# Kernel tuning notes

Hardware: AMD Instinct MI355X
Metric: run time of the kernel (lower is better)

Reference implementation:

```python
import jax, jax.numpy as jnp
import numpy as np


def setup_inputs() -> dict:
    key = jax.random.key(0)
    k1, k2, k3 = jax.random.split(key, 3)
    B, H, W, C, Q = 32, 64, 64, 256, 4
    h = jax.random.normal(k1, (B, H, W, C), dtype=jnp.float32)
    mask = jax.random.randint(k2, (B, H, W), 0, 2) == 1  # True = masked out
    queries = jax.random.normal(k3, (Q, C), dtype=jnp.float32)
    return {"h": h, "mask": mask, "queries": queries}


def reference(h, mask, queries):
    B, H, W, C = h.shape
    Q = queries.shape[0]
    scale = C ** (-0.5)
    h_flat = h.reshape(B, H * W, C)            # [B, N, C]
    # scores: [B, Q, N]
    attn = jnp.einsum('qc,bnc->bqn', queries, h_flat) * scale
    mask_flat = mask.reshape(B, 1, H * W)      # True -> -inf
    attn = jnp.where(mask_flat, -jnp.inf, attn)
    attn = jax.nn.softmax(attn, axis=-1)
    attn = jnp.where(jnp.isnan(attn), 0.0, attn)  # nan_to_num for fully-masked rows
    pooled = jnp.einsum('bqn,bnc->bqc', attn, h_flat)
    return pooled.reshape(B, Q * C)
```

## Files before the change

### kernel.cpp

```cpp
#include <hip/hip_runtime.h>
#include <math.h>

#define QN  4
#define CN  256
#define BN  32
#define NN  4096
#define WV  4
#define RPW 64
#define TR  8
#define NT  8
#define SPB 16

#define LOADT(tt) do {                                                   \
    _Pragma("unroll")                                                    \
    for (int j_ = 0; j_ < TR; ++j_) {                                    \
        const int rw_ = (tt) * TR + j_;                                  \
        if (!((mbits >> rw_) & 1ull))                                    \
            vst[j_] = *(const float4*)(hb + (size_t)rw_ * CN + lane * 4);\
        else                                                             \
            vst[j_] = make_float4(0.f, 0.f, 0.f, 0.f);                   \
    }                                                                    \
} while (0)

#define STORET(bp) do {                                                  \
    _Pragma("unroll")                                                    \
    for (int j_ = 0; j_ < TR; ++j_)                                      \
        *(float4*)((bp) + j_ * CN + lane * 4) = vst[j_];                 \
} while (0)

__global__ __launch_bounds__(256) void k_fused(
    const float* __restrict__ h, const int* __restrict__ mask,
    const float* __restrict__ qr,
    float* __restrict__ P, float* __restrict__ L)
{
    __shared__ float  s_stage[WV][2][TR * CN];
    __shared__ float4 s_pb[WV][TR];
    __shared__ float  s_lp[WV][QN];

    const int b    = blockIdx.x >> 4;
    const int sub  = blockIdx.x & (SPB - 1);
    const int w    = threadIdx.x >> 6;
    const int lane = threadIdx.x & 63;
    const int rgrp = lane >> 4;
    const int l15  = lane & 15;

    const int n0    = (sub * WV + w) * RPW;
    const size_t gn = (size_t)b * NN + n0;
    const float* __restrict__ hb = h + gn * CN;

    float4 q4[QN][4];
#pragma unroll
    for (int q = 0; q < QN; ++q)
#pragma unroll
        for (int k = 0; k < 4; ++k) {
            float4 t = *(const float4*)(qr + q * CN + (l15 + 16 * k) * 4);
            t.x *= 0.0625f; t.y *= 0.0625f; t.z *= 0.0625f; t.w *= 0.0625f;
            q4[q][k] = t;
        }

    const unsigned long long mbits = __ballot(mask[gn + lane] != 0);

    float* const buf0 = &s_stage[w][0][0];
    float* const buf1 = &s_stage[w][1][0];

    float4 acc[QN];
    float  lsum[QN];
#pragma unroll
    for (int q = 0; q < QN; ++q) {
        acc[q] = make_float4(0.f, 0.f, 0.f, 0.f);
        lsum[q] = 0.f;
    }

    float4 vst[TR];

    LOADT(0);
    STORET(buf0);
    LOADT(1);

    for (int t = 0; t < NT; ++t) {
        float* const bufc = (t & 1) ? buf1 : buf0;
        float* const bufn = (t & 1) ? buf0 : buf1;

#pragma unroll
        for (int sp = 0; sp < 2; ++sp) {
            const int rt = sp * 4 + rgrp;
            const float* rowp = bufc + rt * CN;
            float s0 = 0.f, s1 = 0.f, s2 = 0.f, s3 = 0.f;
#pragma unroll
            for (int k = 0; k < 4; ++k) {
                const float4 hv = *(const float4*)(rowp + (l15 + 16 * k) * 4);
                s0 += hv.x * q4[0][k].x + hv.y * q4[0][k].y
                    + hv.z * q4[0][k].z + hv.w * q4[0][k].w;
                s1 += hv.x * q4[1][k].x + hv.y * q4[1][k].y
                    + hv.z * q4[1][k].z + hv.w * q4[1][k].w;
                s2 += hv.x * q4[2][k].x + hv.y * q4[2][k].y
                    + hv.z * q4[2][k].z + hv.w * q4[2][k].w;
                s3 += hv.x * q4[3][k].x + hv.y * q4[3][k].y
                    + hv.z * q4[3][k].z + hv.w * q4[3][k].w;
            }
#pragma unroll
            for (int off = 1; off <= 8; off <<= 1) {
                s0 += __shfl_xor(s0, off, 64);
                s1 += __shfl_xor(s1, off, 64);
                s2 += __shfl_xor(s2, off, 64);
                s3 += __shfl_xor(s3, off, 64);
            }
            const bool mk = ((mbits >> (t * TR + rt)) & 1ull) != 0;
            float4 pv;
            pv.x = mk ? 0.f : __expf(s0);
            pv.y = mk ? 0.f : __expf(s1);
            pv.z = mk ? 0.f : __expf(s2);
            pv.w = mk ? 0.f : __expf(s3);
            if (l15 == 0) s_pb[w][rt] = pv;
        }

#pragma unroll
        for (int r = 0; r < TR; ++r) {
            const float4 pv = s_pb[w][r];
            const float4 hv = *(const float4*)(bufc + r * CN + lane * 4);
            acc[0].x += pv.x * hv.x; acc[0].y += pv.x * hv.y;
            acc[0].z += pv.x * hv.z; acc[0].w += pv.x * hv.w;
            acc[1].x += pv.y * hv.x; acc[1].y += pv.y * hv.y;
            acc[1].z += pv.y * hv.z; acc[1].w += pv.y * hv.w;
            acc[2].x += pv.z * hv.x; acc[2].y += pv.z * hv.y;
            acc[2].z += pv.z * hv.z; acc[2].w += pv.z * hv.w;
            acc[3].x += pv.w * hv.x; acc[3].y += pv.w * hv.y;
            acc[3].z += pv.w * hv.z; acc[3].w += pv.w * hv.w;
            lsum[0] += pv.x; lsum[1] += pv.y;
            lsum[2] += pv.z; lsum[3] += pv.w;
        }

        if (t + 1 < NT) {
            STORET(bufn);
            if (t + 2 < NT) LOADT(t + 2);
        }
    }

    {
        float* part = &s_stage[w][0][0];
#pragma unroll
        for (int q = 0; q < QN; ++q)
            *(float4*)(part + q * CN + lane * 4) = acc[q];
        if (lane == 0) {
#pragma unroll
            for (int q = 0; q < QN; ++q) s_lp[w][q] = lsum[q];
        }
    }
    __syncthreads();
    {
        const int t = threadIdx.x;
        float4 o = make_float4(0.f, 0.f, 0.f, 0.f);
#pragma unroll
        for (int ww = 0; ww < WV; ++ww) {
            const float4 v = *(const float4*)(&s_stage[ww][0][0] + t * 4);
            o.x += v.x; o.y += v.y; o.z += v.z; o.w += v.w;
        }
        ((float4*)(P + (size_t)blockIdx.x * (QN * CN)))[t] = o;
        if (t < QN)
            L[blockIdx.x * QN + t] =
                s_lp[0][t] + s_lp[1][t] + s_lp[2][t] + s_lp[3][t];
    }
}

__global__ __launch_bounds__(256) void k_div(
    const float* __restrict__ P, const float* __restrict__ L,
    float* __restrict__ out)
{
    const int b = blockIdx.x;
    const int t = threadIdx.x;
    const int q = t >> 6;

    float4 o = make_float4(0.f, 0.f, 0.f, 0.f);
    float  l = 0.f;
#pragma unroll 4
    for (int s = 0; s < SPB; ++s) {
        const float4 pv =
            ((const float4*)(P + (size_t)(b * SPB + s) * (QN * CN)))[t];
        o.x += pv.x; o.y += pv.y; o.z += pv.z; o.w += pv.w;
        l += L[(b * SPB + s) * QN + q];
    }
    const float inv = (l > 0.f) ? 1.f / l : 0.f;
    o.x *= inv; o.y *= inv; o.z *= inv; o.w *= inv;
    ((float4*)(out + (size_t)b * (QN * CN)))[t] = o;
}

extern "C" void kernel_launch(void* const* d_in, const int* in_sizes, int n_in,
                              void* d_out, int out_size, void* d_ws, size_t ws_size,
                              hipStream_t stream) {
    const float* h    = (const float*)d_in[0];
    const int*   mask = (const int*)d_in[1];
    const float* qr   = (const float*)d_in[2];
    float*       out  = (float*)d_out;

    float* P = (float*)d_ws;
    float* L = P + (size_t)BN * SPB * QN * CN;

    k_fused<<<BN * SPB, 256, 0, stream>>>(h, mask, qr, P, L);
    k_div  <<<BN, 256, 0, stream>>>(P, L, out);
}
```

Baseline: 28.52 us.

## Double split count, halve rows per wave, and use transpose-reduce shuffles

Halves rows per wave and tile height while doubling blocks per batch, so the grid grows from 512 to 1024 blocks and more waves can be resident to hide memory latency. The four-query butterfly reduction becomes a transpose-style reduction that needs fewer shuffles, with each lane writing one probability. The divide kernel is split per query, giving 128 blocks instead of 32. The cost is twice as many partial results in the workspace, which the second kernel must read and sum.

After: 51.26 us. +79.8%, slower.

```diff
diff --git a/kernel.cpp b/kernel.cpp
--- a/kernel.cpp
+++ b/kernel.cpp
@@ -6,10 +6,10 @@
 #define BN  32
 #define NN  4096
 #define WV  4
-#define RPW 64
-#define TR  8
+#define RPW 32
+#define TR  4
 #define NT  8
-#define SPB 16
+#define SPB 32
 
 #define LOADT(tt) do {                                                   \
     _Pragma("unroll")                                                    \
@@ -28,21 +28,22 @@
         *(float4*)((bp) + j_ * CN + lane * 4) = vst[j_];                 \
 } while (0)
 
-__global__ __launch_bounds__(256) void k_fused(
+__global__ __launch_bounds__(256, 4) void k_fused(
     const float* __restrict__ h, const int* __restrict__ mask,
     const float* __restrict__ qr,
     float* __restrict__ P, float* __restrict__ L)
 {
-    __shared__ float  s_stage[WV][2][TR * CN];
-    __shared__ float4 s_pb[WV][TR];
-    __shared__ float  s_lp[WV][QN];
+    __shared__ float s_stage[WV][2][TR * CN];
+    __shared__ float s_pbf[WV][TR * QN];
+    __shared__ float s_lp[WV][QN];
 
-    const int b    = blockIdx.x >> 4;
+    const int b    = blockIdx.x >> 5;
     const int sub  = blockIdx.x & (SPB - 1);
     const int w    = threadIdx.x >> 6;
     const int lane = threadIdx.x & 63;
     const int rgrp = lane >> 4;
     const int l15  = lane & 15;
+    const int bit0 = l15 & 1, bit1 = (l15 >> 1) & 1;
 
     const int n0    = (sub * WV + w) * RPW;
     const size_t gn = (size_t)b * NN + n0;
@@ -58,7 +59,8 @@
             q4[q][k] = t;
         }
 
-    const unsigned long long mbits = __ballot(mask[gn + lane] != 0);
+    const unsigned long long mbits =
+        __ballot(lane < RPW ? (mask[gn + lane] != 0) : true);
 
     float* const buf0 = &s_stage[w][0][0];
     float* const buf1 = &s_stage[w][1][0];
@@ -81,10 +83,8 @@
         float* const bufc = (t & 1) ? buf1 : buf0;
         float* const bufn = (t & 1) ? buf0 : buf1;
 
-#pragma unroll
-        for (int sp = 0; sp < 2; ++sp) {
-            const int rt = sp * 4 + rgrp;
-            const float* rowp = bufc + rt * CN;
+        {
+            const float* rowp = bufc + rgrp * CN;
             float s0 = 0.f, s1 = 0.f, s2 = 0.f, s3 = 0.f;
 #pragma unroll
             for (int k = 0; k < 4; ++k) {
@@ -98,25 +98,27 @@
                 s3 += hv.x * q4[3][k].x + hv.y * q4[3][k].y
                     + hv.z * q4[3][k].z + hv.w * q4[3][k].w;
             }
-#pragma unroll
-            for (int off = 1; off <= 8; off <<= 1) {
-                s0 += __shfl_xor(s0, off, 64);
-                s1 += __shfl_xor(s1, off, 64);
-                s2 += __shfl_xor(s2, off, 64);
-                s3 += __shfl_xor(s3, off, 64);
-            }
-            const bool mk = ((mbits >> (t * TR + rt)) & 1ull) != 0;
-            float4 pv;
-            pv.x = mk ? 0.f : __expf(s0);
-            pv.y = mk ? 0.f : __expf(s1);
-            pv.z = mk ? 0.f : __expf(s2);
-            pv.w = mk ? 0.f : __expf(s3);
-            if (l15 == 0) s_pb[w][rt] = pv;
+            float t0 = bit0 ? s0 : s2;
+            float t1 = bit0 ? s1 : s3;
+            float r0 = __shfl_xor(t0, 1, 64);
+            float r1 = __shfl_xor(t1, 1, 64);
+            float a0 = (bit0 ? s2 : s0) + r0;
+            float a1 = (bit0 ? s3 : s1) + r1;
+            float tb = bit1 ? a0 : a1;
+            float rb = __shfl_xor(tb, 2, 64);
+            float bq = (bit1 ? a1 : a0) + rb;
+            bq += __shfl_xor(bq, 4, 64);
+            bq += __shfl_xor(bq, 8, 64);
+
+            const bool mk = ((mbits >> (t * TR + rgrp)) & 1ull) != 0;
+            const float p = mk ? 0.f : __expf(bq);
+            if (l15 < 4)
+                s_pbf[w][rgrp * QN + 2 * bit0 + bit1] = p;
         }
 
 #pragma unroll
         for (int r = 0; r < TR; ++r) {
-            const float4 pv = s_pb[w][r];
+            const float4 pv = *(const float4*)&s_pbf[w][r * QN];
             const float4 hv = *(const float4*)(bufc + r * CN + lane * 4);
             acc[0].x += pv.x * hv.x; acc[0].y += pv.x * hv.y;
             acc[0].z += pv.x * hv.z; acc[0].w += pv.x * hv.w;
@@ -166,22 +168,17 @@
     const float* __restrict__ P, const float* __restrict__ L,
     float* __restrict__ out)
 {
-    const int b = blockIdx.x;
-    const int t = threadIdx.x;
-    const int q = t >> 6;
+    const int b   = blockIdx.x >> 2;
+    const int q   = blockIdx.x & 3;
+    const int idx = q * CN + threadIdx.x;
 
-    float4 o = make_float4(0.f, 0.f, 0.f, 0.f);
-    float  l = 0.f;
+    float o = 0.f, l = 0.f;
 #pragma unroll 4
     for (int s = 0; s < SPB; ++s) {
-        const float4 pv =
-            ((const float4*)(P + (size_t)(b * SPB + s) * (QN * CN)))[t];
-        o.x += pv.x; o.y += pv.y; o.z += pv.z; o.w += pv.w;
+        o += P[(size_t)(b * SPB + s) * (QN * CN) + idx];
         l += L[(b * SPB + s) * QN + q];
     }
-    const float inv = (l > 0.f) ? 1.f / l : 0.f;
-    o.x *= inv; o.y *= inv; o.z *= inv; o.w *= inv;
-    ((float4*)(out + (size_t)b * (QN * CN)))[t] = o;
+    out[(size_t)b * (QN * CN) + idx] = (l > 0.f) ? o / l : 0.f;
 }
 
 extern "C" void kernel_launch(void* const* d_in, const int* in_sizes, int n_in,
@@ -196,5 +193,5 @@
     float* L = P + (size_t)BN * SPB * QN * CN;
 
     k_fused<<<BN * SPB, 256, 0, stream>>>(h, mask, qr, P, L);
-    k_div  <<<BN, 256, 0, stream>>>(P, L, out);
+    k_div  <<<BN * QN, 256, 0, stream>>>(P, L, out);
 }
```
